# Kernel tuning notes

Hardware: AMD Instinct MI355X
Metric: run time of the kernel (lower is better)

## Reference

```python
import jax, jax.numpy as jnp
import numpy as np

N_NODES = 20000   # atoms
N_EDGES = 320000  # bonds = line-graph nodes
N_ANGLES = 640000 # line-graph edges
N_GRAPHS = 256
NF = 92           # node_features
EF = 40           # edge_features (= RBF/ABF bins)
FC = 256
LAYERS = 3


def _bn(x, g, b):
    # BatchNorm1d in training mode: batch stats, biased variance, eps=1e-5
    mu = jnp.mean(x, axis=0)
    var = jnp.var(x, axis=0)
    return g * (x - mu) * jax.lax.rsqrt(var + 1e-5) + b


def _rbf(x, vmin, vmax, bins):
    centers = jnp.linspace(vmin, vmax, bins)
    gamma = 1.0 / (centers[1] - centers[0])  # 1/lengthscale (ALIGNN RBFExpansion)
    return jnp.exp(-gamma * (x[:, None] - centers) ** 2)


def _conv(src, dst, n_nodes, nf, ef, Ws, bs, Wd, bd, We, be, gm, bm, gn, bn2):
    # CGCNN conv: gather(u_add_v) + edge linear + BN + gated act + scatter-sum + BN + softplus residual
    h_src = nf @ Ws + bs                       # [N, 2F]
    h_dst = nf @ Wd + bd                       # [N, 2F]
    m = h_src[src] + h_dst[dst] + ef @ We + be # [E, 2F]
    m = _bn(m, gm, bm)
    h_f, h_s = jnp.split(m, 2, axis=1)
    m = jax.nn.sigmoid(h_f) * jax.nn.softplus(h_s)          # [E, F]
    h = jax.ops.segment_sum(m, dst, num_segments=n_nodes)   # scatter-sum to dst nodes
    h = _bn(h, gn, bn2)
    return jax.nn.softplus(nf + h)


def setup_inputs() -> dict:
    key = jax.random.key(0)
    ks = iter(jax.random.split(key, 64))
    rn = lambda *s: jax.random.normal(next(ks), s, dtype=jnp.float32)
    d = {}
    d['atom_features'] = rn(N_NODES, NF)
    d['r'] = rn(N_EDGES, 3) * 2.0  # bond vectors; norms land within RBF range [0, 8]
    d['angle_h'] = ((jax.random.uniform(next(ks), (N_ANGLES,), dtype=jnp.float32) - 0.5) * np.pi)
    d['g_src'] = jax.random.randint(next(ks), (N_EDGES,), 0, N_NODES, dtype=jnp.int32)
    d['g_dst'] = jax.random.randint(next(ks), (N_EDGES,), 0, N_NODES, dtype=jnp.int32)
    d['lg_src'] = jax.random.randint(next(ks), (N_ANGLES,), 0, N_EDGES, dtype=jnp.int32)
    d['lg_dst'] = jax.random.randint(next(ks), (N_ANGLES,), 0, N_EDGES, dtype=jnp.int32)
    d['node_gid'] = jnp.sort(jax.random.randint(next(ks), (N_NODES,), 0, N_GRAPHS, dtype=jnp.int32))
    d['emb_W'] = rn(NF, NF) * 0.1
    d['emb_b'] = jnp.zeros((NF,), jnp.float32)
    # conv layers on atom graph: node dim NF, edge dim EF, out 2*NF
    d['c1_Wsrc'] = rn(LAYERS, NF, 2 * NF) * 0.1
    d['c1_bsrc'] = jnp.zeros((LAYERS, 2 * NF), jnp.float32)
    d['c1_Wdst'] = rn(LAYERS, NF, 2 * NF) * 0.1
    d['c1_bdst'] = jnp.zeros((LAYERS, 2 * NF), jnp.float32)
    d['c1_Wedge'] = rn(LAYERS, EF, 2 * NF) * 0.1
    d['c1_bedge'] = jnp.zeros((LAYERS, 2 * NF), jnp.float32)
    d['c1_bnm_g'] = jnp.ones((LAYERS, 2 * NF), jnp.float32)
    d['c1_bnm_b'] = jnp.zeros((LAYERS, 2 * NF), jnp.float32)
    d['c1_bn_g'] = jnp.ones((LAYERS, NF), jnp.float32)
    d['c1_bn_b'] = jnp.zeros((LAYERS, NF), jnp.float32)
    # conv layers on line graph: node dim EF, edge dim EF, out 2*EF
    d['c2_Wsrc'] = rn(LAYERS, EF, 2 * EF) * 0.1
    d['c2_bsrc'] = jnp.zeros((LAYERS, 2 * EF), jnp.float32)
    d['c2_Wdst'] = rn(LAYERS, EF, 2 * EF) * 0.1
    d['c2_bdst'] = jnp.zeros((LAYERS, 2 * EF), jnp.float32)
    d['c2_Wedge'] = rn(LAYERS, EF, 2 * EF) * 0.1
    d['c2_bedge'] = jnp.zeros((LAYERS, 2 * EF), jnp.float32)
    d['c2_bnm_g'] = jnp.ones((LAYERS, 2 * EF), jnp.float32)
    d['c2_bnm_b'] = jnp.zeros((LAYERS, 2 * EF), jnp.float32)
    d['c2_bn_g'] = jnp.ones((LAYERS, EF), jnp.float32)
    d['c2_bn_b'] = jnp.zeros((LAYERS, EF), jnp.float32)
    d['fc_W'] = rn(NF, FC) * 0.1
    d['fc_b'] = jnp.zeros((FC,), jnp.float32)
    d['out_W'] = rn(FC, 1) * 0.1
    d['out_b'] = jnp.zeros((1,), jnp.float32)
    return d


def reference(atom_features, r, angle_h, g_src, g_dst, lg_src, lg_dst, node_gid,
              emb_W, emb_b,
              c1_Wsrc, c1_bsrc, c1_Wdst, c1_bdst, c1_Wedge, c1_bedge,
              c1_bnm_g, c1_bnm_b, c1_bn_g, c1_bn_b,
              c2_Wsrc, c2_bsrc, c2_Wdst, c2_bdst, c2_Wedge, c2_bedge,
              c2_bnm_g, c2_bnm_b, c2_bn_g, c2_bn_b,
              fc_W, fc_b, out_W, out_b):
    angle_features = _rbf(angle_h, -np.pi / 2, np.pi / 2, EF)      # [E2, EF]
    bondlength = jnp.linalg.norm(r, axis=1)                        # [E]
    edge_features = _rbf(bondlength, 0.0, 8.0, EF)                 # [E, EF]
    node_features = atom_features @ emb_W + emb_b                  # [N, NF]
    for i in range(LAYERS):
        node_features = _conv(g_src, g_dst, N_NODES, node_features, edge_features,
                              c1_Wsrc[i], c1_bsrc[i], c1_Wdst[i], c1_bdst[i],
                              c1_Wedge[i], c1_bedge[i], c1_bnm_g[i], c1_bnm_b[i],
                              c1_bn_g[i], c1_bn_b[i])
        edge_features = _conv(lg_src, lg_dst, N_EDGES, edge_features, angle_features,
                              c2_Wsrc[i], c2_bsrc[i], c2_Wdst[i], c2_bdst[i],
                              c2_Wedge[i], c2_bedge[i], c2_bnm_g[i], c2_bnm_b[i],
                              c2_bn_g[i], c2_bn_b[i])
    # AvgPooling readout over nodes per graph
    sums = jax.ops.segment_sum(node_features, node_gid, num_segments=N_GRAPHS)
    cnts = jax.ops.segment_sum(jnp.ones((N_NODES,), node_features.dtype), node_gid, num_segments=N_GRAPHS)
    feats = sums / jnp.maximum(cnts, 1.0)[:, None]                 # [G, NF]
    feats = jax.nn.softplus(feats)
    feats = jax.nn.softplus(feats @ fc_W + fc_b)                   # fc = Linear + Softplus, then extra softplus
    feats = jax.nn.softplus(feats)
    out = feats @ out_W + out_b                                    # [G, 1], link = identity
    return jnp.squeeze(out, axis=-1)                               # [G]
```

## Files before the change

### kernel.cpp

```cpp
#include <hip/hip_runtime.h>
#include <math.h>

#define N_NODES   20000
#define N_EDGESC  320000
#define N_ANGLESC 640000
#define N_GRAPHSC 256
#define NFDIM     92
#define EFDIM     40
#define FCDIM     256

typedef unsigned short u16;
typedef unsigned int u32;
typedef __attribute__((ext_vector_type(8))) short bf16x8;
typedef __attribute__((ext_vector_type(4))) float f32x4;

__device__ __forceinline__ u16 f2bf(float x) {
  union { float f; unsigned u; } v; v.f = x;
  unsigned r = v.u + 0x7fff + ((v.u >> 16) & 1);
  return (u16)(r >> 16);
}
__device__ __forceinline__ float bf2f(u16 h) {
  union { unsigned u; float f; } v; v.u = ((unsigned)h) << 16; return v.f;
}
__device__ __forceinline__ u32 pk2(float a, float b) {
  return (u32)f2bf(a) | ((u32)f2bf(b) << 16);
}
__device__ __forceinline__ float fsp(float x) {
  float e = __expf(-fabsf(x));
  return fmaxf(x, 0.f) + __logf(1.f + e);
}
__device__ __forceinline__ float fsig(float x) {
  float e = __expf(-x);
  return __builtin_amdgcn_rcpf(1.f + e);
}

__global__ void k_hist(const int* __restrict__ dst, int E, int* __restrict__ hist) {
  int e = blockIdx.x * blockDim.x + threadIdx.x;
  if (e < E) atomicAdd(&hist[dst[e]], 1);
}

__global__ void k_scan_pass1(const int* __restrict__ hist, int n, int* __restrict__ bsum) {
  __shared__ int buf[256];
  int i = blockIdx.x * 256 + threadIdx.x;
  buf[threadIdx.x] = (i < n) ? hist[i] : 0;
  __syncthreads();
  for (int o = 128; o > 0; o >>= 1) {
    if (threadIdx.x < o) buf[threadIdx.x] += buf[threadIdx.x + o];
    __syncthreads();
  }
  if (threadIdx.x == 0) bsum[blockIdx.x] = buf[0];
}

__global__ void k_scan_partials(int* __restrict__ bsum, int B) {
  __shared__ int buf[256];
  __shared__ int carry;
  if (threadIdx.x == 0) carry = 0;
  __syncthreads();
  for (int base = 0; base < B; base += 256) {
    int i = base + threadIdx.x;
    int v = (i < B) ? bsum[i] : 0;
    buf[threadIdx.x] = v;
    __syncthreads();
    for (int o = 1; o < 256; o <<= 1) {
      int t = (threadIdx.x >= o) ? buf[threadIdx.x - o] : 0;
      __syncthreads();
      buf[threadIdx.x] += t;
      __syncthreads();
    }
    if (i < B) bsum[i] = buf[threadIdx.x] - v + carry;
    int tile_total = buf[255];
    __syncthreads();
    if (threadIdx.x == 0) carry += tile_total;
    __syncthreads();
  }
}

__global__ void k_scan_pass3(const int* __restrict__ hist, int n, int total,
                             const int* __restrict__ bsum,
                             int* __restrict__ offsets, int* __restrict__ cursor) {
  __shared__ int buf[256];
  int i = blockIdx.x * 256 + threadIdx.x;
  int v = (i < n) ? hist[i] : 0;
  buf[threadIdx.x] = v;
  __syncthreads();
  for (int o = 1; o < 256; o <<= 1) {
    int t = (threadIdx.x >= o) ? buf[threadIdx.x - o] : 0;
    __syncthreads();
    buf[threadIdx.x] += t;
    __syncthreads();
  }
  int excl = buf[threadIdx.x] - v + bsum[blockIdx.x];
  if (i < n) {
    offsets[i] = excl;
    cursor[i] = excl;
    if (i == n - 1) offsets[n] = total;
  }
}

__global__ void k_fill(const int* __restrict__ dst, int E,
                       int* __restrict__ cursor, int* __restrict__ perm) {
  int e = blockIdx.x * blockDim.x + threadIdx.x;
  if (e >= E) return;
  int pos = atomicAdd(&cursor[dst[e]], 1);
  perm[pos] = e;
}

__global__ void k_sortbins(const int* __restrict__ offsets, int* __restrict__ perm, int nb) {
  int n = blockIdx.x * blockDim.x + threadIdx.x;
  if (n >= nb) return;
  int lo = offsets[n], hi = offsets[n + 1];
  for (int i = lo + 1; i < hi; i++) {
    int key = perm[i];
    int j = i - 1;
    while (j >= lo && perm[j] > key) { perm[j + 1] = perm[j]; j--; }
    perm[j + 1] = key;
  }
}

__global__ void k_invperm(const int* __restrict__ perm, int E, int* __restrict__ iperm) {
  int p = blockIdx.x * blockDim.x + threadIdx.x;
  if (p < E) iperm[perm[p]] = p;
}

__global__ void k_rbf_edge(const float* __restrict__ r, u16* __restrict__ ef) {
  int e = blockIdx.x * blockDim.x + threadIdx.x;
  if (e >= N_EDGESC) return;
  float x = r[e * 3 + 0], y = r[e * 3 + 1], z = r[e * 3 + 2];
  float bl = sqrtf(x * x + y * y + z * z);
  const float step = 8.f / 39.f;
  const float g = 39.f / 8.f;
  u32* o = (u32*)(ef + (long long)e * EFDIM);
#pragma unroll
  for (int i = 0; i < 20; i++) {
    float d0 = bl - (2 * i + 0) * step;
    float d1 = bl - (2 * i + 1) * step;
    o[i] = pk2(__expf(-g * d0 * d0), __expf(-g * d1 * d1));
  }
}

__global__ void k_gemm_bias(const float* __restrict__ A, const float* __restrict__ W,
                            const float* __restrict__ b, float* __restrict__ C,
                            int M, int N, int K) {
  int idx = blockIdx.x * blockDim.x + threadIdx.x;
  int total = M * N;
  if (idx >= total) return;
  int row = idx / N, col = idx - row * N;
  const float* a = A + (long long)row * K;
  float acc = b[col];
#pragma unroll 4
  for (int k = 0; k < K; k++) acc += a[k] * W[k * N + col];
  C[idx] = acc;
}

__global__ void k_nf2b(const float* __restrict__ NF, u16* __restrict__ NFb) {
  int idx = blockIdx.x * blockDim.x + threadIdx.x;
  if (idx >= N_NODES * 96) return;
  int n = idx / 96, c = idx - n * 96;
  NFb[idx] = (c < 92) ? f2bf(NF[(long long)n * 92 + c]) : (u16)0;
}

__global__ void k_mkwt1f(const float* __restrict__ Wsrc, const float* __restrict__ bsrc,
                         const float* __restrict__ Wdst, const float* __restrict__ bdst,
                         const float* __restrict__ We, const float* __restrict__ be,
                         u16* __restrict__ WT1F) {
  int idx = blockIdx.x * blockDim.x + threadIdx.x;
  if (idx >= 32 * 192 * 8) return;
  int j = idx & 7;
  int qc = idx >> 3;
  int c = qc % 192;
  int q = qc / 192;
  int k = q * 8 + j;
  float v = 0.f;
  if (c < 184) {
    if (k < 92) v = Wsrc[k * 184 + c];
    else if (k >= 96 && k < 188) v = Wdst[(k - 96) * 184 + c];
    else if (k >= 192 && k < 232) v = We[(k - 192) * 184 + c];
    else if (k == 232) v = bsrc[c] + bdst[c] + be[c];
  }
  WT1F[idx] = f2bf(v);
}

__global__ void k_mkwt2(const float* __restrict__ Ws, const float* __restrict__ bs,
                        const float* __restrict__ Wd, const float* __restrict__ bd,
                        const float* __restrict__ We, const float* __restrict__ be,
                        u16* __restrict__ WT2) {
  int idx = blockIdx.x * blockDim.x + threadIdx.x;
  if (idx >= 80 * 128) return;
  int c = idx >> 7, k = idx & 127;
  float v = 0.f;
  if (k < 40) v = Ws[k * 80 + c];
  else if (k < 80) v = Wd[(k - 40) * 80 + c];
  else if (k < 120) v = We[(k - 80) * 80 + c];
  else if (k == 120) v = bs[c] + bd[c] + be[c];
  int b = 2 * k;
  int off = c * 256 + (((b >> 4) ^ (c & 7)) << 4) + (b & 15);
  WT2[off >> 1] = f2bf(v);
}

__global__ __launch_bounds__(256) void k_conv1_mfma2(
    const u16* __restrict__ NFb, const u16* __restrict__ EF,
    const int* __restrict__ src, const int* __restrict__ dst,
    const u16* __restrict__ WT1F, const int* __restrict__ IPERM,
    u16* __restrict__ M, float* __restrict__ PART) {
  __shared__ __align__(16) char sA[64 * 512];
  __shared__ __align__(16) char sBc[4 * 192 * 16];
  __shared__ float ssum[2][192];
  __shared__ int srcs[64], dsts[64], ipm[64];
  int t = threadIdx.x;
  int e0 = blockIdx.x * 64;
  for (int i = t; i < 2 * 192; i += 256) ((float*)ssum)[i] = 0.f;
  if (t < 64) {
    srcs[t] = src[e0 + t];
    dsts[t] = dst[e0 + t];
    ipm[t] = IPERM[e0 + t];
  }
  __syncthreads();
  int lane = t & 63, w = t >> 6;
  {
    int r = lane;
    if (w == 0) {
      const uint4* g = (const uint4*)(NFb + (long long)srcs[r] * 96);
#pragma unroll
      for (int ch = 0; ch < 12; ch++)
        *(uint4*)(sA + r * 512 + ((ch ^ (r & 7)) << 4)) = g[ch];
    } else if (w == 1) {
      const uint4* g = (const uint4*)(NFb + (long long)dsts[r] * 96);
#pragma unroll
      for (int ch = 0; ch < 12; ch++)
        *(uint4*)(sA + r * 512 + (((ch + 12) ^ (r & 7)) << 4)) = g[ch];
    } else if (w == 2) {
      const uint4* g = (const uint4*)(EF + (long long)(e0 + r) * 40);
#pragma unroll
      for (int ch = 0; ch < 5; ch++)
        *(uint4*)(sA + r * 512 + (((ch + 24) ^ (r & 7)) << 4)) = g[ch];
    } else {
      uint4 zb = {0x00003F80u, 0u, 0u, 0u};
      uint4 z = {0u, 0u, 0u, 0u};
      *(uint4*)(sA + r * 512 + ((29 ^ (r & 7)) << 4)) = zb;
      *(uint4*)(sA + r * 512 + ((30 ^ (r & 7)) << 4)) = z;
      *(uint4*)(sA + r * 512 + ((31 ^ (r & 7)) << 4)) = z;
    }
  }
  int lr = lane & 15, lg = lane >> 4;
  int arow = w * 16 + lr;
  f32x4 zero = {0.f, 0.f, 0.f, 0.f};
  f32x4 acc[12];
#pragma unroll
  for (int n = 0; n < 12; n++) acc[n] = zero;
  const uint4* wsrc4 = (const uint4*)WT1F;
  for (int kt = 0; kt < 8; kt++) {
    __syncthreads();
    {
      uint4* bb = (uint4*)sBc;
      int base = kt * 768;
#pragma unroll
      for (int i = 0; i < 3; i++) bb[t + i * 256] = wsrc4[base + t + i * 256];
    }
    __syncthreads();
    int q = kt * 4 + lg;
    bf16x8 a = *(const bf16x8*)(sA + arow * 512 + ((q ^ (arow & 7)) << 4));
#pragma unroll
    for (int n = 0; n < 12; n++) {
      bf16x8 b = *(const bf16x8*)(sBc + ((lg * 192 + n * 16 + lr) << 4));
      acc[n] = __builtin_amdgcn_mfma_f32_16x16x32_bf16(a, b, acc[n], 0, 0, 0);
    }
  }
  __syncthreads();
  u16* stage = (u16*)sA;
  int base_r = w * 16 + lg * 4;
#pragma unroll
  for (int n = 0; n < 12; n++) {
    int col = n * 16 + lr;
    bool valid = col < 184;
    int pos = (col < 92) ? (2 * col) : (2 * (col - 92) + 1);
    float s = 0.f, q2 = 0.f;
#pragma unroll
    for (int j = 0; j < 4; j++) {
      float v = acc[n][j];
      if (valid) {
        stage[(base_r + j) * 196 + pos] = f2bf(v);
        s += v; q2 += v * v;
      }
    }
    s += __shfl_xor(s, 16, 64); s += __shfl_xor(s, 32, 64);
    q2 += __shfl_xor(q2, 16, 64); q2 += __shfl_xor(q2, 32, 64);
    if (valid && lg == 0) {
      atomicAdd(&ssum[0][col], s);
      atomicAdd(&ssum[1][col], q2);
    }
  }
  __syncthreads();
  for (int i = t; i < 64 * 46; i += 256) {
    int rr = i / 46, ch = i - rr * 46;
    *(uint2*)(M + (long long)ipm[rr] * 184 + ch * 4) = *(const uint2*)(stage + rr * 196 + ch * 4);
  }
  float* P = PART + (long long)blockIdx.x * 368;
  for (int i = t; i < 184; i += 256) { P[i] = ssum[0][i]; P[184 + i] = ssum[1][i]; }
}

__global__ __launch_bounds__(256) void k_conv2_mfma(
    const u16* __restrict__ EF, const float* __restrict__ angle_h,
    const int* __restrict__ lsrc, const int* __restrict__ ldst,
    const u16* __restrict__ WT2, const int* __restrict__ IPERM,
    u16* __restrict__ M, float* __restrict__ PART) {
  __shared__ __align__(16) char sA[64 * 256];
  __shared__ __align__(16) char sB[80 * 256];
  __shared__ float ssum[2][80];
  __shared__ int srcl[64], dstl[64], ipm[64];
  __shared__ float hh[64];
  int t = threadIdx.x;
  int a0 = blockIdx.x * 64;
  if (t < 64) {
    srcl[t] = lsrc[a0 + t]; dstl[t] = ldst[a0 + t];
    hh[t] = angle_h[a0 + t]; ipm[t] = IPERM[a0 + t];
  }
  for (int i = t; i < 160; i += 256) ((float*)ssum)[i] = 0.f;
  __syncthreads();
  int lane = t & 63, w = t >> 6;
  if (w == 0) {
    int r = lane;
    const uint4* g = (const uint4*)EF + (long long)srcl[r] * 5;
#pragma unroll
    for (int ch = 0; ch < 5; ch++)
      *(uint4*)(sA + r * 256 + ((ch ^ (r & 7)) << 4)) = g[ch];
  } else if (w == 1) {
    int r = lane;
    const uint4* g = (const uint4*)EF + (long long)dstl[r] * 5;
#pragma unroll
    for (int ch = 0; ch < 5; ch++)
      *(uint4*)(sA + r * 256 + (((ch + 5) ^ (r & 7)) << 4)) = g[ch];
  } else {
    int r = lane;
    const float PI = 3.14159265358979323846f;
    const float step = PI / 39.f;
    const float gam = 39.f / PI;
    float h = hh[r];
    int k0 = (w == 2) ? 0 : 20;
#pragma unroll
    for (int p = 0; p < 10; p++) {
      int k = k0 + 2 * p;
      float d0 = h - (-PI * 0.5f + k * step);
      float d1 = h - (-PI * 0.5f + (k + 1) * step);
      u32 val = pk2(__expf(-gam * d0 * d0), __expf(-gam * d1 * d1));
      int b = 160 + 2 * k;
      *(u32*)(sA + r * 256 + (((b >> 4) ^ (r & 7)) << 4) + (b & 15)) = val;
    }
    if (w == 3) {
      uint4 z15 = {0x00003F80u, 0u, 0u, 0u};
      *(uint4*)(sA + r * 256 + ((15 ^ (r & 7)) << 4)) = z15;
    }
  }
  {
    const uint4* wg = (const uint4*)WT2;
    uint4* bb = (uint4*)sB;
    for (int i = t; i < 1280; i += 256) bb[i] = wg[i];
  }
  __syncthreads();

  int lr = lane & 15, lg = lane >> 4;
  int arow = w * 16 + lr;
  f32x4 zero = {0.f, 0.f, 0.f, 0.f};
  f32x4 acc[5];
#pragma unroll
  for (int n = 0; n < 5; n++) acc[n] = zero;
#pragma unroll
  for (int kt = 0; kt < 4; kt++) {
    bf16x8 a = *(const bf16x8*)(sA + arow * 256 + (((kt * 4 + lg) ^ (arow & 7)) << 4));
#pragma unroll
    for (int n = 0; n < 5; n++) {
      int brow = n * 16 + lr;
      bf16x8 b = *(const bf16x8*)(sB + brow * 256 + (((kt * 4 + lg) ^ (brow & 7)) << 4));
      acc[n] = __builtin_amdgcn_mfma_f32_16x16x32_bf16(a, b, acc[n], 0, 0, 0);
    }
  }
  __syncthreads();
  u16* stage = (u16*)sB;
  int base_r = w * 16 + lg * 4;
#pragma unroll
  for (int n = 0; n < 5; n++) {
    int col = n * 16 + lr;
    int pos = (col < 40) ? (2 * col) : (2 * (col - 40) + 1);
    float s = 0.f, q = 0.f;
#pragma unroll
    for (int j = 0; j < 4; j++) {
      float v = acc[n][j];
      stage[(base_r + j) * 80 + pos] = f2bf(v);
      s += v; q += v * v;
    }
    s += __shfl_xor(s, 16, 64); s += __shfl_xor(s, 32, 64);
    q += __shfl_xor(q, 16, 64); q += __shfl_xor(q, 32, 64);
    if (lg == 0) {
      atomicAdd(&ssum[0][col], s);
      atomicAdd(&ssum[1][col], q);
    }
  }
  __syncthreads();
  for (int i = t; i < 64 * 10; i += 256) {
    int rr = i / 10, ch = i - rr * 10;
    *(uint4*)(M + (long long)ipm[rr] * 80 + ch * 8) = *(const uint4*)(stage + rr * 80 + ch * 8);
  }
  float* P = PART + (long long)blockIdx.x * 160;
  for (int i = t; i < 80; i += 256) { P[i] = ssum[0][i]; P[80 + i] = ssum[1][i]; }
}

__global__ __launch_bounds__(256) void k_reduce_part(
    const float* __restrict__ part, int nblk, int C2, float* __restrict__ stat) {
  int chunks = gridDim.x;
  int per = (nblk + chunks - 1) / chunks;
  int lo = blockIdx.x * per;
  int hi = lo + per; if (hi > nblk) hi = nblk;
  if (lo >= hi) return;
  for (int c = threadIdx.x; c < C2; c += blockDim.x) {
    float s = 0.f;
    for (int b = lo; b < hi; b++) s += part[(long long)b * C2 + c];
    atomicAdd(&stat[c], s);
  }
}

__global__ void k_finalize(float* __restrict__ stat, const float* __restrict__ g,
                           const float* __restrict__ b, float* __restrict__ scsh,
                           int C, float invR) {
  int c = threadIdx.x + blockIdx.x * blockDim.x;
  if (c >= C) return;
  float mu = stat[c] * invR;
  float var = stat[C + c] * invR - mu * mu;
  float is = rsqrtf(var + 1e-5f);
  float sc = g[c] * is;
  scsh[c] = sc;
  scsh[C + c] = b[c] - mu * sc;
  stat[c] = 0.f;
  stat[C + c] = 0.f;
}

__global__ __launch_bounds__(512) void k_gather1(
    const u16* __restrict__ m, const int* __restrict__ offsets,
    const float* __restrict__ scsh, float* __restrict__ hagg, float* __restrict__ part) {
  __shared__ float sacc[4][92];
  int t = threadIdx.x;
  int ln = t >> 7, c = t & 127;
  int n = blockIdx.x * 4 + ln;
  if (c < 92) {
    float sc_f = scsh[c],       sh_f = scsh[184 + c];
    float sc_s = scsh[92 + c],  sh_s = scsh[276 + c];
    int lo = offsets[n], hi = offsets[n + 1];
    float acc = 0.f;
    for (int p = lo; p < hi; ++p) {
      u32 pr = *(const u32*)(m + (long long)p * 184 + 2 * c);
      float mf = bf2f((u16)(pr & 0xffffu)) * sc_f + sh_f;
      float ms = bf2f((u16)(pr >> 16)) * sc_s + sh_s;
      acc += fsig(mf) * fsp(ms);
    }
    hagg[(long long)n * 92 + c] = acc;
    sacc[ln][c] = acc;
  }
  __syncthreads();
  if (t < 184) {
    int cc = (t < 92) ? t : t - 92;
    bool sq = t >= 92;
    float s = 0.f;
#pragma unroll
    for (int b = 0; b < 4; b++) { float v = sacc[b][cc]; s += sq ? v * v : v; }
    part[(long long)blockIdx.x * 184 + t] = s;
  }
}

__global__ __launch_bounds__(320) void k_gather2(
    const u16* __restrict__ m, const int* __restrict__ offsets,
    const float* __restrict__ scsh, u16* __restrict__ hagg, float* __restrict__ part) {
  __shared__ float sacc[8][40];
  int t = threadIdx.x;
  int le = t / 40, c = t - le * 40;
  int e = blockIdx.x * 8 + le;
  float sc_f = scsh[c],      sh_f = scsh[80 + c];
  float sc_s = scsh[40 + c], sh_s = scsh[120 + c];
  int lo = offsets[e], hi = offsets[e + 1];
  float acc = 0.f;
  for (int p = lo; p < hi; ++p) {
    u32 pr = *(const u32*)(m + (long long)p * 80 + 2 * c);
    float mf = bf2f((u16)(pr & 0xffffu)) * sc_f + sh_f;
    float ms = bf2f((u16)(pr >> 16)) * sc_s + sh_s;
    acc += fsig(mf) * fsp(ms);
  }
  hagg[(long long)e * 40 + c] = f2bf(acc);
  sacc[le][c] = acc;
  __syncthreads();
  if (t < 80) {
    int cc = (t < 40) ? t : t - 40;
    bool sq = t >= 40;
    float s = 0.f;
#pragma unroll
    for (int b = 0; b < 8; b++) { float v = sacc[b][cc]; s += sq ? v * v : v; }
    part[(long long)blockIdx.x * 80 + t] = s;
  }
}

__global__ void k_bn_residual(const float* __restrict__ xin, const float* __restrict__ hagg,
                              const float* __restrict__ scsh, float* __restrict__ out,
                              int total, int C) {
  int idx = blockIdx.x * blockDim.x + threadIdx.x;
  if (idx >= total) return;
  int c = idx % C;
  out[idx] = fsp(xin[idx] + hagg[idx] * scsh[c] + scsh[C + c]);
}

__global__ void k_bn_residual_bb(u16* __restrict__ ef, const u16* __restrict__ hagg,
                                 const float* __restrict__ scsh, int total, int C) {
  int idx = blockIdx.x * blockDim.x + threadIdx.x;
  if (idx >= total) return;
  int c = idx % C;
  float v = fsp(bf2f(ef[idx]) + bf2f(hagg[idx]) * scsh[c] + scsh[C + c]);
  ef[idx] = f2bf(v);
}

__global__ __launch_bounds__(256) void k_head(
    const float* __restrict__ nf, const int* __restrict__ gid,
    const float* __restrict__ fcW, const float* __restrict__ fcb,
    const float* __restrict__ outW, const float* __restrict__ outb,
    float* __restrict__ out) {
  __shared__ float feats[NFDIM];
  __shared__ float warpsum[4];
  int g = blockIdx.x, t = threadIdx.x;
  int lo = 0, hi = N_NODES;
  while (lo < hi) { int mid = (lo + hi) >> 1; if (gid[mid] < g) lo = mid + 1; else hi = mid; }
  int lo2 = lo, hi2 = N_NODES;
  while (lo2 < hi2) { int mid = (lo2 + hi2) >> 1; if (gid[mid] < g + 1) lo2 = mid + 1; else hi2 = mid; }
  if (t < NFDIM) {
    float s = 0.f;
    for (int n = lo; n < lo2; ++n) s += nf[(long long)n * NFDIM + t];
    float cgt = fmaxf((float)(lo2 - lo), 1.f);
    feats[t] = fsp(s / cgt);
  }
  __syncthreads();
  float acc = fcb[t];
#pragma unroll 4
  for (int k = 0; k < NFDIM; k++) acc += feats[k] * fcW[k * FCDIM + t];
  float z = fsp(fsp(acc));
  float v = z * outW[t];
  for (int off = 32; off > 0; off >>= 1) v += __shfl_down(v, off, 64);
  if ((t & 63) == 0) warpsum[t >> 6] = v;
  __syncthreads();
  if (t == 0) out[g] = warpsum[0] + warpsum[1] + warpsum[2] + warpsum[3] + outb[0];
}

__global__ void k_sentinel(float* out, float v) {
  int i = blockIdx.x * blockDim.x + threadIdx.x;
  if (i < N_GRAPHSC) out[i] = v;
}

static inline int cdiv(long long a, long long b) { return (int)((a + b - 1) / b); }

extern "C" void kernel_launch(void* const* d_in, const int* in_sizes, int n_in,
                              void* d_out, int out_size, void* d_ws, size_t ws_size,
                              hipStream_t stream) {
  (void)in_sizes; (void)n_in; (void)out_size;
  const float* atom_features = (const float*)d_in[0];
  const float* r             = (const float*)d_in[1];
  const float* angle_h       = (const float*)d_in[2];
  const int*   g_src         = (const int*)d_in[3];
  const int*   g_dst         = (const int*)d_in[4];
  const int*   lg_src        = (const int*)d_in[5];
  const int*   lg_dst        = (const int*)d_in[6];
  const int*   node_gid      = (const int*)d_in[7];
  const float* emb_W         = (const float*)d_in[8];
  const float* emb_b         = (const float*)d_in[9];
  const float* c1_Wsrc       = (const float*)d_in[10];
  const float* c1_bsrc       = (const float*)d_in[11];
  const float* c1_Wdst       = (const float*)d_in[12];
  const float* c1_bdst       = (const float*)d_in[13];
  const float* c1_Wedge      = (const float*)d_in[14];
  const float* c1_bedge      = (const float*)d_in[15];
  const float* c1_bnm_g      = (const float*)d_in[16];
  const float* c1_bnm_b      = (const float*)d_in[17];
  const float* c1_bn_g       = (const float*)d_in[18];
  const float* c1_bn_b       = (const float*)d_in[19];
  const float* c2_Wsrc       = (const float*)d_in[20];
  const float* c2_bsrc       = (const float*)d_in[21];
  const float* c2_Wdst       = (const float*)d_in[22];
  const float* c2_bdst       = (const float*)d_in[23];
  const float* c2_Wedge      = (const float*)d_in[24];
  const float* c2_bedge      = (const float*)d_in[25];
  const float* c2_bnm_g      = (const float*)d_in[26];
  const float* c2_bnm_b      = (const float*)d_in[27];
  const float* c2_bn_g       = (const float*)d_in[28];
  const float* c2_bn_b       = (const float*)d_in[29];
  const float* fc_W          = (const float*)d_in[30];
  const float* fc_b          = (const float*)d_in[31];
  const float* out_W         = (const float*)d_in[32];
  const float* out_b         = (const float*)d_in[33];

  char* basep = (char*)d_ws;
  size_t off = 0;
  auto walloc = [&](size_t bytes) {
    char* p = basep + off;
    off += (bytes + 255) & ~(size_t)255;
    return p;
  };
  u16*   M     = (u16*)walloc((size_t)58880000 * 2);
  u16*   EF    = (u16*)walloc((size_t)12800000 * 2);
  float* NF    = (float*)walloc((size_t)1840000 * 4);
  u16*   NFb   = (u16*)walloc((size_t)20000 * 96 * 2);
  float* HAGG1 = (float*)walloc((size_t)1840000 * 4);
  u16*   HAGG2 = (u16*)walloc((size_t)12800000 * 2);
  float* PART  = (float*)walloc((size_t)3200000 * 4);
  int*   HIST  = (int*)walloc((size_t)320000 * 4);
  int*   OFF1  = (int*)walloc((size_t)20001 * 4);
  int*   CUR1  = (int*)walloc((size_t)20000 * 4);
  int*   PERM1 = (int*)walloc((size_t)320000 * 4);
  int*   IPERM1= (int*)walloc((size_t)320000 * 4);
  int*   OFF2  = (int*)walloc((size_t)320001 * 4);
  int*   CUR2  = (int*)walloc((size_t)320000 * 4);
  int*   PERM2 = (int*)walloc((size_t)640000 * 4);
  int*   IPERM2= (int*)walloc((size_t)640000 * 4);
  int*   BSUM  = (int*)walloc((size_t)2048 * 4);
  u16*   WT1F  = (u16*)walloc((size_t)32 * 192 * 8 * 2);
  u16*   WT2   = (u16*)walloc((size_t)80 * 128 * 2);
  float* STAT  = (float*)walloc(512 * 4);
  float* SCSHM = (float*)walloc(1024 * 4);
  float* SCSHN = (float*)walloc(512 * 4);
  if (ws_size < off) {
    k_sentinel<<<1, 256, 0, stream>>>((float*)d_out, (float)(ws_size >> 20));
    return;
  }

  hipMemsetAsync(STAT, 0, 512 * sizeof(float), stream);

  {
    int NB = N_NODES, E = N_EDGESC;
    int B = cdiv(NB, 256);
    hipMemsetAsync(HIST, 0, (size_t)NB * 4, stream);
    k_hist<<<cdiv(E, 256), 256, 0, stream>>>(g_dst, E, HIST);
    k_scan_pass1<<<B, 256, 0, stream>>>(HIST, NB, BSUM);
    k_scan_partials<<<1, 256, 0, stream>>>(BSUM, B);
    k_scan_pass3<<<B, 256, 0, stream>>>(HIST, NB, E, BSUM, OFF1, CUR1);
    k_fill<<<cdiv(E, 256), 256, 0, stream>>>(g_dst, E, CUR1, PERM1);
    k_sortbins<<<cdiv(NB, 256), 256, 0, stream>>>(OFF1, PERM1, NB);
    k_invperm<<<cdiv(E, 256), 256, 0, stream>>>(PERM1, E, IPERM1);
  }
  {
    int NB = N_EDGESC, E = N_ANGLESC;
    int B = cdiv(NB, 256);
    hipMemsetAsync(HIST, 0, (size_t)NB * 4, stream);
    k_hist<<<cdiv(E, 256), 256, 0, stream>>>(lg_dst, E, HIST);
    k_scan_pass1<<<B, 256, 0, stream>>>(HIST, NB, BSUM);
    k_scan_partials<<<1, 256, 0, stream>>>(BSUM, B);
    k_scan_pass3<<<B, 256, 0, stream>>>(HIST, NB, E, BSUM, OFF2, CUR2);
    k_fill<<<cdiv(E, 256), 256, 0, stream>>>(lg_dst, E, CUR2, PERM2);
    k_sortbins<<<cdiv(NB, 256), 256, 0, stream>>>(OFF2, PERM2, NB);
    k_invperm<<<cdiv(E, 256), 256, 0, stream>>>(PERM2, E, IPERM2);
  }

  k_rbf_edge<<<cdiv(N_EDGESC, 256), 256, 0, stream>>>(r, EF);
  k_gemm_bias<<<cdiv((long long)N_NODES * NFDIM, 256), 256, 0, stream>>>(
      atom_features, emb_W, emb_b, NF, N_NODES, NFDIM, NFDIM);
  k_nf2b<<<cdiv((long long)N_NODES * 96, 256), 256, 0, stream>>>(NF, NFb);

  for (int i = 0; i < 3; i++) {
    k_mkwt1f<<<cdiv(32 * 192 * 8, 256), 256, 0, stream>>>(
        c1_Wsrc + i * NFDIM * 2 * NFDIM, c1_bsrc + i * 2 * NFDIM,
        c1_Wdst + i * NFDIM * 2 * NFDIM, c1_bdst + i * 2 * NFDIM,
        c1_Wedge + i * EFDIM * 2 * NFDIM, c1_bedge + i * 2 * NFDIM, WT1F);
    k_conv1_mfma2<<<N_EDGESC / 64, 256, 0, stream>>>(NFb, EF, g_src, g_dst, WT1F, IPERM1, M, PART);
    k_reduce_part<<<256, 256, 0, stream>>>(PART, N_EDGESC / 64, 368, STAT);
    k_finalize<<<1, 256, 0, stream>>>(STAT, c1_bnm_g + i * 184, c1_bnm_b + i * 184, SCSHM, 184, 1.f / N_EDGESC);
    k_gather1<<<N_NODES / 4, 512, 0, stream>>>(M, OFF1, SCSHM, HAGG1, PART);
    k_reduce_part<<<256, 256, 0, stream>>>(PART, N_NODES / 4, 184, STAT);
    k_finalize<<<1, 256, 0, stream>>>(STAT, c1_bn_g + i * 92, c1_bn_b + i * 92, SCSHN, 92, 1.f / N_NODES);
    k_bn_residual<<<cdiv((long long)N_NODES * NFDIM, 256), 256, 0, stream>>>(
        NF, HAGG1, SCSHN, NF, N_NODES * NFDIM, NFDIM);
    k_nf2b<<<cdiv((long long)N_NODES * 96, 256), 256, 0, stream>>>(NF, NFb);

    k_mkwt2<<<40, 256, 0, stream>>>(
        c2_Wsrc + i * EFDIM * 2 * EFDIM, c2_bsrc + i * 2 * EFDIM,
        c2_Wdst + i * EFDIM * 2 * EFDIM, c2_bdst + i * 2 * EFDIM,
        c2_Wedge + i * EFDIM * 2 * EFDIM, c2_bedge + i * 2 * EFDIM, WT2);
    k_conv2_mfma<<<N_ANGLESC / 64, 256, 0, stream>>>(EF, angle_h, lg_src, lg_dst, WT2, IPERM2, M, PART);
    k_reduce_part<<<256, 256, 0, stream>>>(PART, N_ANGLESC / 64, 160, STAT);
    k_finalize<<<1, 256, 0, stream>>>(STAT, c2_bnm_g + i * 80, c2_bnm_b + i * 80, SCSHM, 80, 1.f / N_ANGLESC);
    k_gather2<<<N_EDGESC / 8, 320, 0, stream>>>(M, OFF2, SCSHM, HAGG2, PART);
    k_reduce_part<<<256, 256, 0, stream>>>(PART, N_EDGESC / 8, 80, STAT);
    k_finalize<<<1, 256, 0, stream>>>(STAT, c2_bn_g + i * 40, c2_bn_b + i * 40, SCSHN, 40, 1.f / N_EDGESC);
    k_bn_residual_bb<<<cdiv((long long)N_EDGESC * EFDIM, 256), 256, 0, stream>>>(
        EF, HAGG2, SCSHN, N_EDGESC * EFDIM, EFDIM);
  }

  k_head<<<N_GRAPHSC, 256, 0, stream>>>(NF, node_gid, fc_W, fc_b, out_W, out_b, (float*)d_out);
}
```

Before: 1.622 ms.

## Fuse BN stat reduce with finalize, fuse residual with bf16 pack, pad LDS

Merges the partial-sum reduction and BatchNorm finalize into one kernel, using a last-block-done atomic counter so the final block computes scale and shift. Fuses the node residual softplus with the bf16 repacking of node features, dropping one elementwise pass and one launch. Pads the conv1 weight tile in shared memory by two rows per k-group to reduce bank conflicts on B-fragment reads. This removes a dozen small launches per forward pass, at the cost of threadfence and atomic-counter synchronisation and a dependence on the DONE counter being correctly reset.

Result: slower. 1.748 ms (+7.8%).

```diff
diff --git a/kernel.cpp b/kernel.cpp
--- a/kernel.cpp
+++ b/kernel.cpp
@@ -203,7 +203,7 @@
     const u16* __restrict__ WT1F, const int* __restrict__ IPERM,
     u16* __restrict__ M, float* __restrict__ PART) {
   __shared__ __align__(16) char sA[64 * 512];
-  __shared__ __align__(16) char sBc[4 * 192 * 16];
+  __shared__ __align__(16) char sBc[4 * 194 * 16];
   __shared__ float ssum[2][192];
   __shared__ int srcs[64], dsts[64], ipm[64];
   int t = threadIdx.x;
@@ -251,17 +251,20 @@
   for (int kt = 0; kt < 8; kt++) {
     __syncthreads();
     {
-      uint4* bb = (uint4*)sBc;
       int base = kt * 768;
 #pragma unroll
-      for (int i = 0; i < 3; i++) bb[t + i * 256] = wsrc4[base + t + i * 256];
+      for (int i = 0; i < 3; i++) {
+        int idx = t + i * 256;
+        int g = idx / 192, c = idx - g * 192;
+        *(uint4*)(sBc + ((g * 194 + c) << 4)) = wsrc4[base + idx];
+      }
     }
     __syncthreads();
     int q = kt * 4 + lg;
     bf16x8 a = *(const bf16x8*)(sA + arow * 512 + ((q ^ (arow & 7)) << 4));
 #pragma unroll
     for (int n = 0; n < 12; n++) {
-      bf16x8 b = *(const bf16x8*)(sBc + ((lg * 192 + n * 16 + lr) << 4));
+      bf16x8 b = *(const bf16x8*)(sBc + ((lg * 194 + n * 16 + lr) << 4));
       acc[n] = __builtin_amdgcn_mfma_f32_16x16x32_bf16(a, b, acc[n], 0, 0, 0);
     }
   }
@@ -403,33 +406,41 @@
   for (int i = t; i < 80; i += 256) { P[i] = ssum[0][i]; P[80 + i] = ssum[1][i]; }
 }
 
-__global__ __launch_bounds__(256) void k_reduce_part(
-    const float* __restrict__ part, int nblk, int C2, float* __restrict__ stat) {
+__global__ __launch_bounds__(256) void k_reduce_fin(
+    const float* __restrict__ part, int nblk, int C2, float* __restrict__ stat,
+    const float* __restrict__ g, const float* __restrict__ b, float* __restrict__ scsh,
+    int C, float invR, int* __restrict__ done) {
   int chunks = gridDim.x;
   int per = (nblk + chunks - 1) / chunks;
   int lo = blockIdx.x * per;
   int hi = lo + per; if (hi > nblk) hi = nblk;
-  if (lo >= hi) return;
-  for (int c = threadIdx.x; c < C2; c += blockDim.x) {
-    float s = 0.f;
-    for (int b = lo; b < hi; b++) s += part[(long long)b * C2 + c];
-    atomicAdd(&stat[c], s);
-  }
-}
-
-__global__ void k_finalize(float* __restrict__ stat, const float* __restrict__ g,
-                           const float* __restrict__ b, float* __restrict__ scsh,
-                           int C, float invR) {
-  int c = threadIdx.x + blockIdx.x * blockDim.x;
-  if (c >= C) return;
-  float mu = stat[c] * invR;
-  float var = stat[C + c] * invR - mu * mu;
-  float is = rsqrtf(var + 1e-5f);
-  float sc = g[c] * is;
-  scsh[c] = sc;
-  scsh[C + c] = b[c] - mu * sc;
-  stat[c] = 0.f;
-  stat[C + c] = 0.f;
+  if (lo < hi) {
+    for (int c = threadIdx.x; c < C2; c += blockDim.x) {
+      float s = 0.f;
+      for (int bb = lo; bb < hi; bb++) s += part[(long long)bb * C2 + c];
+      atomicAdd(&stat[c], s);
+    }
+  }
+  __threadfence();
+  __shared__ int lastflag;
+  if (threadIdx.x == 0) lastflag = (atomicAdd(done, 1) == (int)gridDim.x - 1) ? 1 : 0;
+  __syncthreads();
+  if (lastflag) {
+    int c = threadIdx.x;
+    if (c < C) {
+      float su = atomicAdd(&stat[c], 0.f);
+      float sq = atomicAdd(&stat[C + c], 0.f);
+      float mu = su * invR;
+      float var = sq * invR - mu * mu;
+      float is = rsqrtf(var + 1e-5f);
+      float sc = g[c] * is;
+      scsh[c] = sc;
+      scsh[C + c] = b[c] - mu * sc;
+      stat[c] = 0.f;
+      stat[C + c] = 0.f;
+    }
+    if (threadIdx.x == 0) *done = 0;
+  }
 }
 
 __global__ __launch_bounds__(512) void k_gather1(
@@ -494,13 +505,15 @@
   }
 }
 
-__global__ void k_bn_residual(const float* __restrict__ xin, const float* __restrict__ hagg,
-                              const float* __restrict__ scsh, float* __restrict__ out,
-                              int total, int C) {
+__global__ void k_bn_residual_nfb(float* __restrict__ NF, const float* __restrict__ hagg,
+                                  const float* __restrict__ scsh, u16* __restrict__ NFb) {
   int idx = blockIdx.x * blockDim.x + threadIdx.x;
-  if (idx >= total) return;
-  int c = idx % C;
-  out[idx] = fsp(xin[idx] + hagg[idx] * scsh[c] + scsh[C + c]);
+  if (idx >= N_NODES * NFDIM) return;
+  int c = idx % NFDIM;
+  float v = fsp(NF[idx] + hagg[idx] * scsh[c] + scsh[NFDIM + c]);
+  NF[idx] = v;
+  int n = idx / NFDIM;
+  NFb[(long long)n * 96 + c] = f2bf(v);
 }
 
 __global__ void k_bn_residual_bb(u16* __restrict__ ef, const u16* __restrict__ hagg,
@@ -615,6 +628,7 @@
   u16*   WT1F  = (u16*)walloc((size_t)32 * 192 * 8 * 2);
   u16*   WT2   = (u16*)walloc((size_t)80 * 128 * 2);
   float* STAT  = (float*)walloc(512 * 4);
+  int*   DONE  = (int*)walloc(256);
   float* SCSHM = (float*)walloc(1024 * 4);
   float* SCSHN = (float*)walloc(512 * 4);
   if (ws_size < off) {
@@ -622,7 +636,7 @@
     return;
   }
 
-  hipMemsetAsync(STAT, 0, 512 * sizeof(float), stream);
+  hipMemsetAsync(STAT, 0, 512 * sizeof(float) + 256, stream);
 
   {
     int NB = N_NODES, E = N_EDGESC;
@@ -660,25 +674,24 @@
         c1_Wdst + i * NFDIM * 2 * NFDIM, c1_bdst + i * 2 * NFDIM,
         c1_Wedge + i * EFDIM * 2 * NFDIM, c1_bedge + i * 2 * NFDIM, WT1F);
     k_conv1_mfma2<<<N_EDGESC / 64, 256, 0, stream>>>(NFb, EF, g_src, g_dst, WT1F, IPERM1, M, PART);
-    k_reduce_part<<<256, 256, 0, stream>>>(PART, N_EDGESC / 64, 368, STAT);
-    k_finalize<<<1, 256, 0, stream>>>(STAT, c1_bnm_g + i * 184, c1_bnm_b + i * 184, SCSHM, 184, 1.f / N_EDGESC);
+    k_reduce_fin<<<256, 256, 0, stream>>>(PART, N_EDGESC / 64, 368, STAT,
+        c1_bnm_g + i * 184, c1_bnm_b + i * 184, SCSHM, 184, 1.f / N_EDGESC, DONE);
     k_gather1<<<N_NODES / 4, 512, 0, stream>>>(M, OFF1, SCSHM, HAGG1, PART);
-    k_reduce_part<<<256, 256, 0, stream>>>(PART, N_NODES / 4, 184, STAT);
-    k_finalize<<<1, 256, 0, stream>>>(STAT, c1_bn_g + i * 92, c1_bn_b + i * 92, SCSHN, 92, 1.f / N_NODES);
-    k_bn_residual<<<cdiv((long long)N_NODES * NFDIM, 256), 256, 0, stream>>>(
-        NF, HAGG1, SCSHN, NF, N_NODES * NFDIM, NFDIM);
-    k_nf2b<<<cdiv((long long)N_NODES * 96, 256), 256, 0, stream>>>(NF, NFb);
+    k_reduce_fin<<<256, 256, 0, stream>>>(PART, N_NODES / 4, 184, STAT,
+        c1_bn_g + i * 92, c1_bn_b + i * 92, SCSHN, 92, 1.f / N_NODES, DONE);
+    k_bn_residual_nfb<<<cdiv((long long)N_NODES * NFDIM, 256), 256, 0, stream>>>(
+        NF, HAGG1, SCSHN, NFb);
 
     k_mkwt2<<<40, 256, 0, stream>>>(
         c2_Wsrc + i * EFDIM * 2 * EFDIM, c2_bsrc + i * 2 * EFDIM,
         c2_Wdst + i * EFDIM * 2 * EFDIM, c2_bdst + i * 2 * EFDIM,
         c2_Wedge + i * EFDIM * 2 * EFDIM, c2_bedge + i * 2 * EFDIM, WT2);
     k_conv2_mfma<<<N_ANGLESC / 64, 256, 0, stream>>>(EF, angle_h, lg_src, lg_dst, WT2, IPERM2, M, PART);
-    k_reduce_part<<<256, 256, 0, stream>>>(PART, N_ANGLESC / 64, 160, STAT);
-    k_finalize<<<1, 256, 0, stream>>>(STAT, c2_bnm_g + i * 80, c2_bnm_b + i * 80, SCSHM, 80, 1.f / N_ANGLESC);
+    k_reduce_fin<<<256, 256, 0, stream>>>(PART, N_ANGLESC / 64, 160, STAT,
+        c2_bnm_g + i * 80, c2_bnm_b + i * 80, SCSHM, 80, 1.f / N_ANGLESC, DONE);
     k_gather2<<<N_EDGESC / 8, 320, 0, stream>>>(M, OFF2, SCSHM, HAGG2, PART);
-    k_reduce_part<<<256, 256, 0, stream>>>(PART, N_EDGESC / 8, 80, STAT);
-    k_finalize<<<1, 256, 0, stream>>>(STAT, c2_bn_g + i * 40, c2_bn_b + i * 40, SCSHN, 40, 1.f / N_EDGESC);
+    k_reduce_fin<<<256, 256, 0, stream>>>(PART, N_EDGESC / 8, 80, STAT,
+        c2_bn_g + i * 40, c2_bn_b + i * 40, SCSHN, 40, 1.f / N_EDGESC, DONE);
     k_bn_residual_bb<<<cdiv((long long)N_EDGESC * EFDIM, 256), 256, 0, stream>>>(
         EF, HAGG2, SCSHN, N_EDGESC * EFDIM, EFDIM);
   }
```

## Split conv1 MFMA work across 8 waves and fuse residual with bf16 pack

Applied to the files above, without the earlier changes.

The conv1 edge GEMM kernel moves from 4 to 8 wavefronts per block. Each wave now gathers half as many rows into shared memory and computes 6 of the 12 output column tiles, so per-thread accumulator registers are halved and more waves are available to hide gather latency. Separately, the node BN-residual kernel now also writes the bf16 padded copy of the node features, which removes the separate conversion launch and one full reread of the fp32 features. The risk is that larger blocks lower block-level occupancy, and that the A fragment is loaded redundantly by two waves.

Result: no change. 1.625 ms (+0.2%).

```diff
diff --git a/kernel.cpp b/kernel.cpp
--- a/kernel.cpp
+++ b/kernel.cpp
@@ -197,7 +197,7 @@
   WT2[off >> 1] = f2bf(v);
 }
 
-__global__ __launch_bounds__(256) void k_conv1_mfma2(
+__global__ __launch_bounds__(512) void k_conv1_mfma2(
     const u16* __restrict__ NFb, const u16* __restrict__ EF,
     const int* __restrict__ src, const int* __restrict__ dst,
     const u16* __restrict__ WT1F, const int* __restrict__ IPERM,
@@ -208,7 +208,7 @@
   __shared__ int srcs[64], dsts[64], ipm[64];
   int t = threadIdx.x;
   int e0 = blockIdx.x * 64;
-  for (int i = t; i < 2 * 192; i += 256) ((float*)ssum)[i] = 0.f;
+  if (t < 384) ((float*)ssum)[t] = 0.f;
   if (t < 64) {
     srcs[t] = src[e0 + t];
     dsts[t] = dst[e0 + t];
@@ -221,56 +221,73 @@
     if (w == 0) {
       const uint4* g = (const uint4*)(NFb + (long long)srcs[r] * 96);
 #pragma unroll
-      for (int ch = 0; ch < 12; ch++)
+      for (int ch = 0; ch < 6; ch++)
         *(uint4*)(sA + r * 512 + ((ch ^ (r & 7)) << 4)) = g[ch];
     } else if (w == 1) {
+      const uint4* g = (const uint4*)(NFb + (long long)srcs[r] * 96);
+#pragma unroll
+      for (int ch = 6; ch < 12; ch++)
+        *(uint4*)(sA + r * 512 + ((ch ^ (r & 7)) << 4)) = g[ch];
+    } else if (w == 2) {
       const uint4* g = (const uint4*)(NFb + (long long)dsts[r] * 96);
 #pragma unroll
-      for (int ch = 0; ch < 12; ch++)
+      for (int ch = 0; ch < 6; ch++)
         *(uint4*)(sA + r * 512 + (((ch + 12) ^ (r & 7)) << 4)) = g[ch];
-    } else if (w == 2) {
+    } else if (w == 3) {
+      const uint4* g = (const uint4*)(NFb + (long long)dsts[r] * 96);
+#pragma unroll
+      for (int ch = 6; ch < 12; ch++)
+        *(uint4*)(sA + r * 512 + (((ch + 12) ^ (r & 7)) << 4)) = g[ch];
+    } else if (w == 4) {
       const uint4* g = (const uint4*)(EF + (long long)(e0 + r) * 40);
 #pragma unroll
-      for (int ch = 0; ch < 5; ch++)
+      for (int ch = 0; ch < 3; ch++)
         *(uint4*)(sA + r * 512 + (((ch + 24) ^ (r & 7)) << 4)) = g[ch];
+    } else if (w == 5) {
+      const uint4* g = (const uint4*)(EF + (long long)(e0 + r) * 40);
+#pragma unroll
+      for (int ch = 3; ch < 5; ch++)
+        *(uint4*)(sA + r * 512 + (((ch + 24) ^ (r & 7)) << 4)) = g[ch];
+    } else if (w == 6) {
+      uint4 zb = {0x00003F80u, 0u, 0u, 0u};
+      *(uint4*)(sA + r * 512 + ((29 ^ (r & 7)) << 4)) = zb;
     } else {
-      uint4 zb = {0x00003F80u, 0u, 0u, 0u};
       uint4 z = {0u, 0u, 0u, 0u};
-      *(uint4*)(sA + r * 512 + ((29 ^ (r & 7)) << 4)) = zb;
       *(uint4*)(sA + r * 512 + ((30 ^ (r & 7)) << 4)) = z;
       *(uint4*)(sA + r * 512 + ((31 ^ (r & 7)) << 4)) = z;
     }
   }
   int lr = lane & 15, lg = lane >> 4;
-  int arow = w * 16 + lr;
+  int rt = w & 3, nh = w >> 2;
+  int arow = rt * 16 + lr;
   f32x4 zero = {0.f, 0.f, 0.f, 0.f};
-  f32x4 acc[12];
-#pragma unroll
-  for (int n = 0; n < 12; n++) acc[n] = zero;
+  f32x4 acc[6];
+#pragma unroll
+  for (int n = 0; n < 6; n++) acc[n] = zero;
   const uint4* wsrc4 = (const uint4*)WT1F;
   for (int kt = 0; kt < 8; kt++) {
     __syncthreads();
     {
-      uint4* bb = (uint4*)sBc;
       int base = kt * 768;
-#pragma unroll
-      for (int i = 0; i < 3; i++) bb[t + i * 256] = wsrc4[base + t + i * 256];
+      *(uint4*)(sBc + (t << 4)) = wsrc4[base + t];
+      if (t < 256) *(uint4*)(sBc + ((512 + t) << 4)) = wsrc4[base + 512 + t];
     }
     __syncthreads();
     int q = kt * 4 + lg;
     bf16x8 a = *(const bf16x8*)(sA + arow * 512 + ((q ^ (arow & 7)) << 4));
 #pragma unroll
-    for (int n = 0; n < 12; n++) {
-      bf16x8 b = *(const bf16x8*)(sBc + ((lg * 192 + n * 16 + lr) << 4));
+    for (int n = 0; n < 6; n++) {
+      int ng = nh * 6 + n;
+      bf16x8 b = *(const bf16x8*)(sBc + ((lg * 192 + ng * 16 + lr) << 4));
       acc[n] = __builtin_amdgcn_mfma_f32_16x16x32_bf16(a, b, acc[n], 0, 0, 0);
     }
   }
   __syncthreads();
   u16* stage = (u16*)sA;
-  int base_r = w * 16 + lg * 4;
-#pragma unroll
-  for (int n = 0; n < 12; n++) {
-    int col = n * 16 + lr;
+  int base_r = rt * 16 + lg * 4;
+#pragma unroll
+  for (int n = 0; n < 6; n++) {
+    int col = (nh * 6 + n) * 16 + lr;
     bool valid = col < 184;
     int pos = (col < 92) ? (2 * col) : (2 * (col - 92) + 1);
     float s = 0.f, q2 = 0.f;
@@ -290,12 +307,12 @@
     }
   }
   __syncthreads();
-  for (int i = t; i < 64 * 46; i += 256) {
+  for (int i = t; i < 64 * 46; i += 512) {
     int rr = i / 46, ch = i - rr * 46;
     *(uint2*)(M + (long long)ipm[rr] * 184 + ch * 4) = *(const uint2*)(stage + rr * 196 + ch * 4);
   }
   float* P = PART + (long long)blockIdx.x * 368;
-  for (int i = t; i < 184; i += 256) { P[i] = ssum[0][i]; P[184 + i] = ssum[1][i]; }
+  if (t < 184) { P[t] = ssum[0][t]; P[184 + t] = ssum[1][t]; }
 }
 
 __global__ __launch_bounds__(256) void k_conv2_mfma(
@@ -494,13 +511,15 @@
   }
 }
 
-__global__ void k_bn_residual(const float* __restrict__ xin, const float* __restrict__ hagg,
-                              const float* __restrict__ scsh, float* __restrict__ out,
-                              int total, int C) {
+__global__ void k_bn_residual_nfb(float* __restrict__ NF, const float* __restrict__ hagg,
+                                  const float* __restrict__ scsh, u16* __restrict__ NFb) {
   int idx = blockIdx.x * blockDim.x + threadIdx.x;
-  if (idx >= total) return;
-  int c = idx % C;
-  out[idx] = fsp(xin[idx] + hagg[idx] * scsh[c] + scsh[C + c]);
+  if (idx >= N_NODES * NFDIM) return;
+  int c = idx % NFDIM;
+  float v = fsp(NF[idx] + hagg[idx] * scsh[c] + scsh[NFDIM + c]);
+  NF[idx] = v;
+  int n = idx / NFDIM;
+  NFb[(long long)n * 96 + c] = f2bf(v);
 }
 
 __global__ void k_bn_residual_bb(u16* __restrict__ ef, const u16* __restrict__ hagg,
@@ -659,15 +678,14 @@
         c1_Wsrc + i * NFDIM * 2 * NFDIM, c1_bsrc + i * 2 * NFDIM,
         c1_Wdst + i * NFDIM * 2 * NFDIM, c1_bdst + i * 2 * NFDIM,
         c1_Wedge + i * EFDIM * 2 * NFDIM, c1_bedge + i * 2 * NFDIM, WT1F);
-    k_conv1_mfma2<<<N_EDGESC / 64, 256, 0, stream>>>(NFb, EF, g_src, g_dst, WT1F, IPERM1, M, PART);
+    k_conv1_mfma2<<<N_EDGESC / 64, 512, 0, stream>>>(NFb, EF, g_src, g_dst, WT1F, IPERM1, M, PART);
     k_reduce_part<<<256, 256, 0, stream>>>(PART, N_EDGESC / 64, 368, STAT);
     k_finalize<<<1, 256, 0, stream>>>(STAT, c1_bnm_g + i * 184, c1_bnm_b + i * 184, SCSHM, 184, 1.f / N_EDGESC);
     k_gather1<<<N_NODES / 4, 512, 0, stream>>>(M, OFF1, SCSHM, HAGG1, PART);
     k_reduce_part<<<256, 256, 0, stream>>>(PART, N_NODES / 4, 184, STAT);
     k_finalize<<<1, 256, 0, stream>>>(STAT, c1_bn_g + i * 92, c1_bn_b + i * 92, SCSHN, 92, 1.f / N_NODES);
-    k_bn_residual<<<cdiv((long long)N_NODES * NFDIM, 256), 256, 0, stream>>>(
-        NF, HAGG1, SCSHN, NF, N_NODES * NFDIM, NFDIM);
-    k_nf2b<<<cdiv((long long)N_NODES * 96, 256), 256, 0, stream>>>(NF, NFb);
+    k_bn_residual_nfb<<<cdiv((long long)N_NODES * NFDIM, 256), 256, 0, stream>>>(
+        NF, HAGG1, SCSHN, NFb);
 
     k_mkwt2<<<40, 256, 0, stream>>>(
         c2_Wsrc + i * EFDIM * 2 * EFDIM, c2_bsrc + i * 2 * EFDIM,
```
